# Optimization experiments

Hardware: AMD Instinct MI355X
Metric: run time of the kernel (lower is better)

## Reference

```python
import jax, jax.numpy as jnp
from jax import lax
import numpy as np

B, T = 64, 1024
N_MELS, ENC, DEC, LSTM, SPK = 80, 256, 128, 512, 256
CTX = ENC + SPK          # encoder_seq feature dim = 512
PRE = 2 * DEC            # prenet fc dims = 256
FILTERS, KS = 32, 31
MAX_R, R = 20, 1         # r buffer initialized to 1
DROP_P = 0.5


def _gru_cell(x, h, w_ih, w_hh, b_ih, b_hh):
    gi = x @ w_ih.T + b_ih
    gh = h @ w_hh.T + b_hh
    i_r, i_z, i_n = jnp.split(gi, 3, axis=-1)
    h_r, h_z, h_n = jnp.split(gh, 3, axis=-1)
    r = jax.nn.sigmoid(i_r + h_r)
    z = jax.nn.sigmoid(i_z + h_z)
    n = jnp.tanh(i_n + r * h_n)
    return (1.0 - z) * n + z * h


def _lstm_cell(x, h, c, w_ih, w_hh, b_ih, b_hh):
    g = x @ w_ih.T + h @ w_hh.T + b_ih + b_hh
    i, f, gg, o = jnp.split(g, 4, axis=-1)
    c2 = jax.nn.sigmoid(f) * c + jax.nn.sigmoid(i) * jnp.tanh(gg)
    h2 = jax.nn.sigmoid(o) * jnp.tanh(c2)
    return h2, c2


def setup_inputs() -> dict:
    key = jax.random.key(0)
    ks = jax.random.split(key, 40)
    n = lambda i, shp: jax.random.normal(ks[i], shp, jnp.float32)
    p = lambda i, shp: jax.random.normal(ks[i], shp, jnp.float32) * 0.05
    return {
        "encoder_seq": n(0, (B, T, CTX)),
        "encoder_seq_proj": n(1, (B, T, DEC)),
        "prenet_in": n(2, (B, N_MELS)),
        "attn_hidden": n(3, (B, DEC)),
        "rnn1_hidden": n(4, (B, LSTM)),
        "rnn2_hidden": n(5, (B, LSTM)),
        "rnn1_cell": n(6, (B, LSTM)),
        "rnn2_cell": n(7, (B, LSTM)),
        "context_vec": n(8, (B, CTX)),
        "chars": jax.random.randint(ks[9], (B, T), 0, 100),
        "t": 0,
        # LSA params (torch layout: Linear weight [out,in])
        "conv_w": p(10, (FILTERS, 1, KS)),
        "conv_b": p(11, (FILTERS,)),
        "L_w": p(12, (DEC, FILTERS)),
        "W_w": p(13, (DEC, DEC)),
        "W_b": p(14, (DEC,)),
        "v_w": p(15, (1, DEC)),
        # PreNet
        "fc1_w": p(16, (PRE, N_MELS)),
        "fc1_b": p(17, (PRE,)),
        "fc2_w": p(18, (PRE, PRE)),
        "fc2_b": p(19, (PRE,)),
        # GRUCell: in = CTX + PRE = 768, hidden = DEC
        "gru_w_ih": p(20, (3 * DEC, CTX + PRE)),
        "gru_w_hh": p(21, (3 * DEC, DEC)),
        "gru_b_ih": p(22, (3 * DEC,)),
        "gru_b_hh": p(23, (3 * DEC,)),
        # rnn_input Linear: CTX + DEC = 640 -> LSTM
        "ri_w": p(24, (LSTM, CTX + DEC)),
        "ri_b": p(25, (LSTM,)),
        # LSTMCells
        "l1_w_ih": p(26, (4 * LSTM, LSTM)),
        "l1_w_hh": p(27, (4 * LSTM, LSTM)),
        "l1_b_ih": p(28, (4 * LSTM,)),
        "l1_b_hh": p(29, (4 * LSTM,)),
        "l2_w_ih": p(30, (4 * LSTM, LSTM)),
        "l2_w_hh": p(31, (4 * LSTM, LSTM)),
        "l2_b_ih": p(32, (4 * LSTM,)),
        "l2_b_hh": p(33, (4 * LSTM,)),
        # output projections
        "mp_w": p(34, (N_MELS * MAX_R, LSTM)),
        "sp_w": p(35, (1, CTX + LSTM)),
        "sp_b": p(36, (1,)),
    }


def reference(encoder_seq, encoder_seq_proj, prenet_in, attn_hidden, rnn1_hidden,
              rnn2_hidden, rnn1_cell, rnn2_cell, context_vec, chars, t,
              conv_w, conv_b, L_w, W_w, W_b, v_w,
              fc1_w, fc1_b, fc2_w, fc2_b,
              gru_w_ih, gru_w_hh, gru_b_ih, gru_b_hh,
              ri_w, ri_b,
              l1_w_ih, l1_w_hh, l1_b_ih, l1_b_hh,
              l2_w_ih, l2_w_hh, l2_b_ih, l2_b_hh,
              mp_w, sp_w, sp_b):
    # PreNet (dropout always on, deterministic keys)
    dk1, dk2 = jax.random.split(jax.random.key(42))
    keep = 1.0 - DROP_P
    h = jax.nn.relu(prenet_in @ fc1_w.T + fc1_b)
    h = h * jax.random.bernoulli(dk1, keep, h.shape).astype(h.dtype) / keep
    h = jax.nn.relu(h @ fc2_w.T + fc2_b)
    prenet_out = h * jax.random.bernoulli(dk2, keep, h.shape).astype(h.dtype) / keep

    # attention GRU
    attn_h = _gru_cell(jnp.concatenate([context_vec, prenet_out], axis=-1),
                       attn_hidden, gru_w_ih, gru_w_hh, gru_b_ih, gru_b_hh)

    # LSA attention at t == 0 (cumulative attention is zeros)
    pq = attn_h @ W_w.T + W_b                              # [B, DEC]
    cumulative = jnp.zeros((B, 1, T), encoder_seq.dtype)
    loc = lax.conv_general_dilated(cumulative, conv_w, (1,), [((KS - 1) // 2,) * 2],
                                   dimension_numbers=("NCH", "OIH", "NCH"))
    loc = loc + conv_b[None, :, None]                      # [B, F, T]
    ploc = jnp.swapaxes(loc, 1, 2) @ L_w.T                 # [B, T, DEC]
    u = (jnp.tanh(pq[:, None, :] + encoder_seq_proj + ploc) @ v_w.T)[..., 0]  # [B, T]
    u = u * (chars != 0).astype(u.dtype)
    scores = jax.nn.softmax(u, axis=1)                     # [B, T]
    context = jnp.einsum("bt,btd->bd", scores, encoder_seq)  # [B, CTX]

    # residual LSTM stack (inference: no zoneout)
    x = jnp.concatenate([context, attn_h], axis=1) @ ri_w.T + ri_b
    h1, c1 = _lstm_cell(x, rnn1_hidden, rnn1_cell, l1_w_ih, l1_w_hh, l1_b_ih, l1_b_hh)
    x = x + h1
    h2, c2 = _lstm_cell(x, rnn2_hidden, rnn2_cell, l2_w_ih, l2_w_hh, l2_b_ih, l2_b_hh)
    x = x + h2

    mels = (x @ mp_w.T).reshape(B, N_MELS, MAX_R)[:, :, :R]  # [B, n_mels, r]
    stop = jax.nn.sigmoid(jnp.concatenate([x, context], axis=1) @ sp_w.T + sp_b)
    return mels, scores[:, None, :], attn_h, h1, h2, c1, c2, context, stop
```

## Files before the change

kernel.cpp:

```cpp
#include <hip/hip_runtime.h>
#include <stdint.h>

#define JAX_PARTITIONABLE 1
#define NB 512

__device__ __forceinline__ float tanh_f(float x) {
  float e = __expf(2.0f * x);
  return 1.0f - 2.0f / (e + 1.0f);
}
__device__ __forceinline__ float sigm(float x) {
  return 1.0f / (1.0f + __expf(-x));
}

__device__ __forceinline__ void stw(float* p, float v) {
  __hip_atomic_store(p, v, __ATOMIC_RELAXED, __HIP_MEMORY_SCOPE_AGENT);
}
__device__ __forceinline__ void stw4(float* p, float4 v) {
  union { float2 f; uint64_t u; } a, b;
  a.f.x = v.x; a.f.y = v.y; b.f.x = v.z; b.f.y = v.w;
  __hip_atomic_store((uint64_t*)p, a.u, __ATOMIC_RELAXED, __HIP_MEMORY_SCOPE_AGENT);
  __hip_atomic_store(((uint64_t*)p) + 1, b.u, __ATOMIC_RELAXED, __HIP_MEMORY_SCOPE_AGENT);
}

__device__ __forceinline__ void tf2x32(unsigned k0, unsigned k1, unsigned x0, unsigned x1,
                                       unsigned &o0, unsigned &o1) {
  unsigned ks0 = k0, ks1 = k1, ks2 = k0 ^ k1 ^ 0x1BD11BDAu;
  x0 += ks0; x1 += ks1;
#define RR(r) { x0 += x1; x1 = (x1 << r) | (x1 >> (32 - r)); x1 ^= x0; }
  RR(13) RR(15) RR(26) RR(6)  x0 += ks1; x1 += ks2 + 1u;
  RR(17) RR(29) RR(16) RR(24) x0 += ks2; x1 += ks0 + 2u;
  RR(13) RR(15) RR(26) RR(6)  x0 += ks0; x1 += ks1 + 3u;
  RR(17) RR(29) RR(16) RR(24) x0 += ks1; x1 += ks2 + 4u;
  RR(13) RR(15) RR(26) RR(6)  x0 += ks2; x1 += ks0 + 5u;
#undef RR
  o0 = x0; o1 = x1;
}

__device__ __forceinline__ float drop_scale(unsigned k0, unsigned k1, unsigned flat) {
#if JAX_PARTITIONABLE
  unsigned o0, o1; tf2x32(k0, k1, 0u, flat, o0, o1);
  unsigned bits = o0 ^ o1;
#else
  unsigned o0, o1, bits;
  if (flat < 8192u) { tf2x32(k0, k1, flat, flat + 8192u, o0, o1); bits = o0; }
  else             { tf2x32(k0, k1, flat - 8192u, flat, o0, o1); bits = o1; }
#endif
  return (bits >> 31) ? 0.0f : 2.0f;
}
__device__ __forceinline__ void get_drop_keys(unsigned &a0, unsigned &a1,
                                              unsigned &b0, unsigned &b1) {
#if JAX_PARTITIONABLE
  tf2x32(0u, 42u, 0u, 0u, a0, a1);
  tf2x32(0u, 42u, 0u, 1u, b0, b1);
#else
  unsigned p0, q0, p1, q1;
  tf2x32(0u, 42u, 0u, 2u, p0, q0);
  tf2x32(0u, 42u, 1u, 3u, p1, q1);
  a0 = p0; a1 = p1; b0 = q0; b1 = q1;
#endif
}

__device__ __forceinline__ void gbar(int* ibase, int phase) {
  __syncthreads();
  if (threadIdx.x == 0) {
    const int s = (int)(blockIdx.x & 15);
    int* sub   = ibase + s * 64;
    int* top   = ibase + 1024;
    int* flags = ibase + 1088;
    int old = __hip_atomic_fetch_add(sub, 1, __ATOMIC_RELAXED, __HIP_MEMORY_SCOPE_AGENT);
    if (old == phase * 32 - 1) {
      int t = __hip_atomic_fetch_add(top, 1, __ATOMIC_RELAXED, __HIP_MEMORY_SCOPE_AGENT);
      if (t == phase * 16 - 1) {
        #pragma unroll
        for (int i = 0; i < 16; i++)
          __hip_atomic_store(flags + i * 64, phase, __ATOMIC_RELAXED, __HIP_MEMORY_SCOPE_AGENT);
      }
    }
    long long guard = 0;
    while (__hip_atomic_load(flags + s * 64, __ATOMIC_RELAXED, __HIP_MEMORY_SCOPE_AGENT) < phase) {
      __builtin_amdgcn_s_sleep(4);
      if (++guard > (1LL << 21)) break;
    }
  }
  __syncthreads();
}

__global__ void k0(int* cnt) {
  for (int i = threadIdx.x; i < 2112; i += 256) cnt[i] = 0;
}

__global__ __launch_bounds__(256, 2) void kM(
    const float* es, const float* esp, const float* prenet_in,
    const float* rnn1_hidden, const float* rnn2_hidden,
    const float* rnn1_cell, const float* rnn2_cell,
    const float* context_vec, const float* attn_hidden, const int* chars,
    const float* conv_b, const float* L_w, const float* W_w, const float* W_b, const float* v_w,
    const float* fc1_w, const float* fc1_b, const float* fc2_w, const float* fc2_b,
    const float* gru_w_ih, const float* gru_w_hh, const float* gru_b_ih, const float* gru_b_hh,
    const float* ri_w, const float* ri_b,
    const float* l1_w_ih, const float* l1_w_hh, const float* l1_b_ih, const float* l1_b_hh,
    const float* l2_w_ih, const float* l2_w_hh, const float* l2_b_ih, const float* l2_b_hh,
    const float* mp_w, const float* sp_w, const float* sp_b,
    float* ws,
    float* mels_o, float* scores_o, float* attn_o, float* h1_o, float* h2_o,
    float* c1_o, float* c2_o, float* ctx_o, float* stop_o) {
  int* ibase = (int*)ws;
  float* pqc    = ws + 2112;
  float* phq    = ws + 2240;
  float* poq    = ws + 18624;
  float* ahq_h  = ws + 35008;
  float* u_buf  = ws + 43200;
  float* ctxq   = ws + 108736;
  float* xq     = ws + 141504;
  float* x2q    = ws + 174272;
  float* x3q    = ws + 207040;
  float* hq1    = ws + 239808;
  float* hq2    = ws + 272576;
  float* cvq    = ws + 305344;
  float* ahq_in = ws + 338112;
  float* c1pT   = ws + 346304;
  float* c2pT   = ws + 379072;

  const float4* cvq4   = (const float4*)cvq;
  const float4* phq4   = (const float4*)phq;
  const float4* poq4   = (const float4*)poq;
  const float4* ahq_in4= (const float4*)ahq_in;
  const float4* ahq_h4 = (const float4*)ahq_h;
  const float4* ctxq4  = (const float4*)ctxq;
  const float4* xq4    = (const float4*)xq;
  const float4* x2q4   = (const float4*)x2q;
  const float4* x3q4   = (const float4*)x3q;
  const float4* hq14   = (const float4*)hq1;
  const float4* hq24   = (const float4*)hq2;

  const int g = blockIdx.x, tid = threadIdx.x;
  const int w = tid >> 6, lane = tid & 63;
  __shared__ float sh[16640];

  if (g < 64) {
    for (int i = tid; i < 5120; i += 256) sh[(i / 80) * 81 + (i % 80)] = prenet_in[i];
    __syncthreads();
    unsigned d1k0, d1k1, d2k0, d2k1;
    get_drop_keys(d1k0, d1k1, d2k0, d2k1);
    const int j = g * 4 + w;
    float acc = fc1_b[j];
    const float* wr = fc1_w + j * 80;
    #pragma unroll 8
    for (int k = 0; k < 80; k += 2) {
      float2 wv = *(const float2*)(wr + k);
      acc += sh[lane * 81 + k] * wv.x + sh[lane * 81 + k + 1] * wv.y;
    }
    acc = fmaxf(acc, 0.0f) * drop_scale(d1k0, d1k1, (unsigned)(lane * 256 + j));
    stw(&phq[g * 256 + lane * 4 + w], acc);
  } else if (g < 96) {
    int t = (g - 64) * 256 + tid;
    int k4 = t >> 6, b = t & 63;
    stw4(&hq1[k4 * 256 + b * 4], ((const float4*)rnn1_hidden)[b * 128 + k4]);
  } else if (g < 128) {
    int t = (g - 96) * 256 + tid;
    int k4 = t >> 6, b = t & 63;
    stw4(&hq2[k4 * 256 + b * 4], ((const float4*)rnn2_hidden)[b * 128 + k4]);
  } else if (g < 160) {
    int t = (g - 128) * 256 + tid;
    int k4 = t >> 6, b = t & 63;
    stw4(&cvq[k4 * 256 + b * 4], ((const float4*)context_vec)[b * 128 + k4]);
  } else if (g < 168) {
    int t = (g - 160) * 256 + tid;
    int k4 = t >> 6, b = t & 63;
    stw4(&ahq_in[k4 * 256 + b * 4], ((const float4*)attn_hidden)[b * 32 + k4]);
  } else if (g < 232) {
    int base = (g - 168) * 512;
    #pragma unroll
    for (int e = 0; e < 2; e++) { int i = base + tid + e * 256; stw(&c1pT[i], rnn1_cell[(i & 63) * 512 + (i >> 6)]); }
  } else if (g < 296) {
    int base = (g - 232) * 512;
    #pragma unroll
    for (int e = 0; e < 2; e++) { int i = base + tid + e * 256; stw(&c2pT[i], rnn2_cell[(i & 63) * 512 + (i >> 6)]); }
  } else if (g < 360) {
    int base = (g - 296) * 512;
    #pragma unroll
    for (int e = 0; e < 2; e++) stw(&ctxq[base + tid + e * 256], 0.0f);
  } else if (g == 360) {
    if (tid < 128) {
      float acc = W_b[tid];
      const float* lw = L_w + tid * 32;
      #pragma unroll
      for (int f = 0; f < 32; f++) acc += conv_b[f] * lw[f];
      stw(&pqc[tid], acc);
    }
  } else {
    const unsigned wi0 = (unsigned)((g - 361) * 256 + tid);
    float acc = 0.0f;
    #pragma unroll
    for (int s = 0; s < 10; s++) acc += es[(size_t)(wi0 + (unsigned)s * 38656u) * 32];
    asm volatile("" :: "v"(acc));
  }
  gbar(ibase, 1);

  if (g < 64) {
    const int j = g * 4 + w;
    ((float4*)(sh + w * 256))[lane] = ((const float4*)(fc2_w + j * 256))[lane];
    __syncthreads();
    unsigned d1k0, d1k1, d2k0, d2k1;
    get_drop_keys(d1k0, d1k1, d2k0, d2k1);
    const float4* wv4 = (const float4*)(sh + w * 256);
    float acc = fc2_b[j];
    #pragma unroll 8
    for (int k4 = 0; k4 < 64; k4++) {
      float4 x4 = phq4[k4 * 64 + lane];
      float4 wv = wv4[k4];
      acc += x4.x * wv.x + x4.y * wv.y + x4.z * wv.z + x4.w * wv.w;
    }
    acc = fmaxf(acc, 0.0f) * drop_scale(d2k0, d2k1, (unsigned)(lane * 256 + j));
    stw(&poq[g * 256 + lane * 4 + w], acc);
  } else {
    const unsigned wi0 = (unsigned)((g - 64) * 256 + tid);
    float acc = 0.0f;
    #pragma unroll
    for (int s = 0; s < 6; s++) {
      unsigned idx = 386560u + wi0 + (unsigned)s * 114688u;
      if (idx < 1048576u) acc += es[(size_t)idx * 32];
    }
    asm volatile("" :: "v"(acc));
  }
  gbar(ibase, 2);

  if (g < 128) {
    if (w < 3) {
      const int rj = g + 128 * w;
      const float4* src = (const float4*)(gru_w_ih + (size_t)rj * 768);
      float4* dst = (float4*)(sh + w * 768);
      #pragma unroll
      for (int q = 0; q < 3; q++) dst[q * 64 + lane] = src[q * 64 + lane];
    } else {
      float4* dst = (float4*)(sh + 2304);
      if (lane < 32) {
        dst[lane]      = ((const float4*)gru_w_hh)[(size_t)g * 32 + lane];
        dst[32 + lane] = ((const float4*)gru_w_hh)[(size_t)(128 + g) * 32 + lane];
        dst[64 + lane] = ((const float4*)gru_w_hh)[(size_t)(256 + g) * 32 + lane];
      }
    }
    __syncthreads();
    if (w < 3) {
      const int rj = g + 128 * w;
      const float4* wv4 = (const float4*)(sh + w * 768);
      float acc = gru_b_ih[rj];
      #pragma unroll 4
      for (int k4 = 0; k4 < 128; k4++) {
        float4 x4 = cvq4[k4 * 64 + lane];
        float4 wv = wv4[k4];
        acc += x4.x * wv.x + x4.y * wv.y + x4.z * wv.z + x4.w * wv.w;
      }
      #pragma unroll 4
      for (int k4 = 0; k4 < 64; k4++) {
        float4 x4 = poq4[k4 * 64 + lane];
        float4 wv = wv4[128 + k4];
        acc += x4.x * wv.x + x4.y * wv.y + x4.z * wv.z + x4.w * wv.w;
      }
      sh[2688 + w * 64 + lane] = acc;
    } else {
      const float4* wh4 = (const float4*)(sh + 2304);
      #pragma unroll
      for (int r = 0; r < 3; r++) {
        float acc = gru_b_hh[r * 128 + g];
        #pragma unroll 4
        for (int k4 = 0; k4 < 32; k4++) {
          float4 x4 = ahq_in4[k4 * 64 + lane];
          float4 wv = wh4[r * 32 + k4];
          acc += x4.x * wv.x + x4.y * wv.y + x4.z * wv.z + x4.w * wv.w;
        }
        sh[2688 + (3 + r) * 64 + lane] = acc;
      }
    }
    __syncthreads();
    if (tid < 64) {
      float gr = sh[2688 + tid]       + sh[2688 + 192 + tid];
      float gz = sh[2688 + 64 + tid]  + sh[2688 + 256 + tid];
      float gin = sh[2688 + 128 + tid];
      float ghn = sh[2688 + 320 + tid];
      float a0 = ahq_in[(g >> 2) * 256 + tid * 4 + (g & 3)];
      float r = sigm(gr), z = sigm(gz);
      float h = (1.0f - z) * tanh_f(gin + r * ghn) + z * a0;
      stw(&ahq_h[(g >> 2) * 256 + tid * 4 + (g & 3)], h);
      attn_o[tid * 128 + g] = h;
    }
  } else {
    const unsigned wi0 = (unsigned)((g - 128) * 256 + tid);
    float acc = 0.0f;
    #pragma unroll
    for (int s = 0; s < 3; s++) {
      unsigned idx = wi0 + (unsigned)s * 98304u;
      if (idx < 262144u) acc += esp[(size_t)idx * 32];
    }
    if (g == 128) { if (tid < 512) acc += W_w[tid * 32]; }
    if (g == 129) {
      #pragma unroll
      for (int s = 0; s < 8; s++) acc += (float)chars[(tid + s * 256) * 32];
    }
    asm volatile("" :: "v"(acc));
  }
  gbar(ibase, 3);

  {
    const int b = g >> 3, tch = g & 7;
    {
      const float4* src = ((const float4*)W_w) + (size_t)(w * 32) * 32;
      float4* dst = (float4*)sh + w * 1024;
      #pragma unroll
      for (int q = 0; q < 16; q++) dst[q * 64 + lane] = src[q * 64 + lane];
    }
    float* pqs = sh + 16384;
    float* shh = sh + 16512;
    if (tid < 128) shh[tid] = ahq_h[(tid >> 2) * 256 + b * 4 + (tid & 3)];
    __syncthreads();
    float2 a2; a2.x = shh[2 * lane]; a2.y = shh[2 * lane + 1];
    for (int ni = 0; ni < 32; ni++) {
      int n = w * 32 + ni;
      float2 wv2 = *(const float2*)(sh + w * 4096 + ni * 128 + 2 * lane);
      float s = a2.x * wv2.x + a2.y * wv2.y;
      for (int off = 32; off > 0; off >>= 1) s += __shfl_xor(s, off, 64);
      if (lane == 0) pqs[n] = s + pqc[n];
    }
    __syncthreads();
    float2 p = *(const float2*)(pqs + 2 * lane);
    float2 v2 = *(const float2*)(v_w + 2 * lane);
    const int tb = tch * 128 + w * 32;
    const float* erow = esp + ((size_t)b * 1024 + tb) * 128 + 2 * lane;
    for (int i2 = 0; i2 < 8; i2++) {
      const float* er = erow + (size_t)i2 * 512;
      float2 e0 = *(const float2*)(er);
      float2 e1 = *(const float2*)(er + 128);
      float2 e2 = *(const float2*)(er + 256);
      float2 e3 = *(const float2*)(er + 384);
      float s0 = v2.x * tanh_f(p.x + e0.x) + v2.y * tanh_f(p.y + e0.y);
      float s1 = v2.x * tanh_f(p.x + e1.x) + v2.y * tanh_f(p.y + e1.y);
      float s2 = v2.x * tanh_f(p.x + e2.x) + v2.y * tanh_f(p.y + e2.y);
      float s3 = v2.x * tanh_f(p.x + e3.x) + v2.y * tanh_f(p.y + e3.y);
      for (int off = 32; off > 0; off >>= 1) {
        s0 += __shfl_down(s0, off, 64);
        s1 += __shfl_down(s1, off, 64);
        s2 += __shfl_down(s2, off, 64);
        s3 += __shfl_down(s3, off, 64);
      }
      if (lane == 0) {
        int t = tb + i2 * 4;
        stw(&u_buf[b * 1024 + t],     (chars[b * 1024 + t]     != 0) ? s0 : 0.0f);
        stw(&u_buf[b * 1024 + t + 1], (chars[b * 1024 + t + 1] != 0) ? s1 : 0.0f);
        stw(&u_buf[b * 1024 + t + 2], (chars[b * 1024 + t + 2] != 0) ? s2 : 0.0f);
        stw(&u_buf[b * 1024 + t + 3], (chars[b * 1024 + t + 3] != 0) ? s3 : 0.0f);
      }
    }
  }
  gbar(ibase, 4);

  {
    const int b = g >> 3, tch = g & 7;
    float* redm = sh;
    float* sc   = sh + 256;
    float* red4 = sh + 384;
    float4 uv = *(const float4*)(u_buf + b * 1024 + tid * 4);
    float m = fmaxf(fmaxf(uv.x, uv.y), fmaxf(uv.z, uv.w));
    redm[tid] = m;
    __syncthreads();
    for (int s = 128; s > 0; s >>= 1) { if (tid < s) redm[tid] = fmaxf(redm[tid], redm[tid + s]); __syncthreads(); }
    float M = redm[0];
    __syncthreads();
    float e0 = __expf(uv.x - M), e1 = __expf(uv.y - M), e2 = __expf(uv.z - M), e3 = __expf(uv.w - M);
    redm[tid] = e0 + e1 + e2 + e3;
    __syncthreads();
    for (int s = 128; s > 0; s >>= 1) { if (tid < s) redm[tid] += redm[tid + s]; __syncthreads(); }
    float inv = 1.0f / redm[0];
    if (tch == 0) {
      float4 r; r.x = e0 * inv; r.y = e1 * inv; r.z = e2 * inv; r.w = e3 * inv;
      *(float4*)(scores_o + b * 1024 + tid * 4) = r;
    }
    if (tid < 128) sc[tid] = __expf(u_buf[b * 1024 + tch * 128 + tid] - M) * inv;
    __syncthreads();
    float acc0 = 0, acc1 = 0, acc2 = 0, acc3 = 0, acc4 = 0, acc5 = 0, acc6 = 0, acc7 = 0;
    const float* base = es + ((size_t)b * 1024 + tch * 128) * 512 + lane * 8;
    for (int i = 0; i < 32; i += 2) {
      int t1 = 4 * i + w, t2 = t1 + 4;
      float4 wa1 = *(const float4*)(base + (size_t)t1 * 512);
      float4 wb1 = *(const float4*)(base + (size_t)t1 * 512 + 4);
      float4 wa2 = *(const float4*)(base + (size_t)t2 * 512);
      float4 wb2 = *(const float4*)(base + (size_t)t2 * 512 + 4);
      float s1 = sc[t1], s2 = sc[t2];
      acc0 += s1 * wa1.x + s2 * wa2.x; acc1 += s1 * wa1.y + s2 * wa2.y;
      acc2 += s1 * wa1.z + s2 * wa2.z; acc3 += s1 * wa1.w + s2 * wa2.w;
      acc4 += s1 * wb1.x + s2 * wb2.x; acc5 += s1 * wb1.y + s2 * wb2.y;
      acc6 += s1 * wb1.z + s2 * wb2.z; acc7 += s1 * wb1.w + s2 * wb2.w;
    }
    float* rr = red4 + w * 512 + lane * 8;
    rr[0] = acc0; rr[1] = acc1; rr[2] = acc2; rr[3] = acc3;
    rr[4] = acc4; rr[5] = acc5; rr[6] = acc6; rr[7] = acc7;
    __syncthreads();
    int d0 = tid * 2;
    float r0 = red4[d0] + red4[512 + d0] + red4[1024 + d0] + red4[1536 + d0];
    float r1 = red4[d0 + 1] + red4[512 + d0 + 1] + red4[1024 + d0 + 1] + red4[1536 + d0 + 1];
    atomicAdd(&ctxq[(d0 >> 2) * 256 + b * 4 + (d0 & 3)], r0);
    atomicAdd(&ctxq[((d0 + 1) >> 2) * 256 + b * 4 + ((d0 + 1) & 3)], r1);
  }
  gbar(ibase, 5);

  {
    const int n = g;
    if (tid < 160) ((float4*)sh)[tid] = ((const float4*)(ri_w + (size_t)n * 640))[tid];
    if (tid < 64) ctx_o[tid * 512 + n] = ctxq[(n >> 2) * 256 + tid * 4 + (n & 3)];
    __syncthreads();
    float acc = 0.0f;
    for (int k4 = w * 40; k4 < w * 40 + 40; k4++) {
      float4 wv = ((float4*)sh)[k4];
      float4 x4 = (k4 < 128) ? ctxq4[k4 * 64 + lane] : ahq_h4[(k4 - 128) * 64 + lane];
      acc += x4.x * wv.x + x4.y * wv.y + x4.z * wv.z + x4.w * wv.w;
    }
    sh[640 + w * 64 + lane] = acc;
    __syncthreads();
    if (tid < 64) stw(&xq[(n >> 2) * 256 + tid * 4 + (n & 3)],
                      ri_b[n] + sh[640 + tid] + sh[704 + tid] + sh[768 + tid] + sh[832 + tid]);
  }
  gbar(ibase, 6);

  {
    const int n = g + (w << 9);
    {
      const float4* si = (const float4*)(l1_w_ih + (size_t)n * 512);
      const float4* sh4 = (const float4*)(l1_w_hh + (size_t)n * 512);
      float4* di = (float4*)sh + w * 256;
      float4* dh = di + 128;
      #pragma unroll
      for (int q = 0; q < 2; q++) { di[q * 64 + lane] = si[q * 64 + lane]; dh[q * 64 + lane] = sh4[q * 64 + lane]; }
    }
    __syncthreads();
    const float4* di = (const float4*)sh + w * 256;
    const float4* dh = di + 128;
    float acc = l1_b_ih[n] + l1_b_hh[n];
    #pragma unroll 4
    for (int k4 = 0; k4 < 128; k4++) {
      float4 x4 = xq4[k4 * 64 + lane];
      float4 wv = di[k4];
      acc += x4.x * wv.x + x4.y * wv.y + x4.z * wv.z + x4.w * wv.w;
    }
    #pragma unroll 4
    for (int k4 = 0; k4 < 128; k4++) {
      float4 x4 = hq14[k4 * 64 + lane];
      float4 wv = dh[k4];
      acc += x4.x * wv.x + x4.y * wv.y + x4.z * wv.z + x4.w * wv.w;
    }
    sh[4096 + w * 64 + lane] = acc;
    __syncthreads();
    if (tid < 64) {
      float gi = sh[4096 + tid], gf = sh[4160 + tid], gg = sh[4224 + tid], go = sh[4288 + tid];
      float c = c1pT[g * 64 + tid];
      float c2 = sigm(gf) * c + sigm(gi) * tanh_f(gg);
      float h2v = sigm(go) * tanh_f(c2);
      h1_o[tid * 512 + g] = h2v;
      c1_o[tid * 512 + g] = c2;
      stw(&x2q[(g >> 2) * 256 + tid * 4 + (g & 3)],
          xq[(g >> 2) * 256 + tid * 4 + (g & 3)] + h2v);
    }
  }
  gbar(ibase, 7);

  {
    const int n = g + (w << 9);
    {
      const float4* si = (const float4*)(l2_w_ih + (size_t)n * 512);
      const float4* sh4 = (const float4*)(l2_w_hh + (size_t)n * 512);
      float4* di = (float4*)sh + w * 256;
      float4* dh = di + 128;
      #pragma unroll
      for (int q = 0; q < 2; q++) { di[q * 64 + lane] = si[q * 64 + lane]; dh[q * 64 + lane] = sh4[q * 64 + lane]; }
    }
    __syncthreads();
    const float4* di = (const float4*)sh + w * 256;
    const float4* dh = di + 128;
    float acc = l2_b_ih[n] + l2_b_hh[n];
    #pragma unroll 4
    for (int k4 = 0; k4 < 128; k4++) {
      float4 x4 = x2q4[k4 * 64 + lane];
      float4 wv = di[k4];
      acc += x4.x * wv.x + x4.y * wv.y + x4.z * wv.z + x4.w * wv.w;
    }
    #pragma unroll 4
    for (int k4 = 0; k4 < 128; k4++) {
      float4 x4 = hq24[k4 * 64 + lane];
      float4 wv = dh[k4];
      acc += x4.x * wv.x + x4.y * wv.y + x4.z * wv.z + x4.w * wv.w;
    }
    sh[4096 + w * 64 + lane] = acc;
    __syncthreads();
    if (tid < 64) {
      float gi = sh[4096 + tid], gf = sh[4160 + tid], gg = sh[4224 + tid], go = sh[4288 + tid];
      float c = c2pT[g * 64 + tid];
      float c2 = sigm(gf) * c + sigm(gi) * tanh_f(gg);
      float h2v = sigm(go) * tanh_f(c2);
      h2_o[tid * 512 + g] = h2v;
      c2_o[tid * 512 + g] = c2;
      stw(&x3q[(g >> 2) * 256 + tid * 4 + (g & 3)],
          x2q[(g >> 2) * 256 + tid * 4 + (g & 3)] + h2v);
    }
  }
  gbar(ibase, 8);

  if (g < 80) {
    const int m = g;
    if (tid < 128) ((float4*)sh)[tid] = ((const float4*)(mp_w + (size_t)m * 20 * 512))[tid];
    __syncthreads();
    float acc = 0.0f;
    for (int k4 = w * 32; k4 < w * 32 + 32; k4++) {
      float4 x4 = x3q4[k4 * 64 + lane];
      float4 wv = ((float4*)sh)[k4];
      acc += x4.x * wv.x + x4.y * wv.y + x4.z * wv.z + x4.w * wv.w;
    }
    sh[512 + w * 64 + lane] = acc;
    __syncthreads();
    if (tid < 64) mels_o[tid * 80 + m] = sh[512 + tid] + sh[576 + tid] + sh[640 + tid] + sh[704 + tid];
  } else if (g == 80) {
    ((float4*)sh)[tid] = ((const float4*)sp_w)[tid];
    __syncthreads();
    float acc = 0.0f;
    for (int k4 = w * 32; k4 < w * 32 + 32; k4++) {
      float4 x4 = x3q4[k4 * 64 + lane];
      float4 c4 = ctxq4[k4 * 64 + lane];
      float4 w1 = ((float4*)sh)[k4];
      float4 w2 = ((float4*)sh)[128 + k4];
      acc += x4.x * w1.x + x4.y * w1.y + x4.z * w1.z + x4.w * w1.w;
      acc += c4.x * w2.x + c4.y * w2.y + c4.z * w2.z + c4.w * w2.w;
    }
    sh[1024 + w * 64 + lane] = acc;
    __syncthreads();
    if (tid < 64) stop_o[tid] = sigm(sp_b[0] + sh[1024 + tid] + sh[1088 + tid] + sh[1152 + tid] + sh[1216 + tid]);
  }
}

extern "C" void kernel_launch(void* const* d_in, const int* in_sizes, int n_in,
                              void* d_out, int out_size, void* d_ws, size_t ws_size,
                              hipStream_t stream) {
  const float* es          = (const float*)d_in[0];
  const float* esp         = (const float*)d_in[1];
  const float* prenet_in   = (const float*)d_in[2];
  const float* attn_hidden = (const float*)d_in[3];
  const float* rnn1_hidden = (const float*)d_in[4];
  const float* rnn2_hidden = (const float*)d_in[5];
  const float* rnn1_cell   = (const float*)d_in[6];
  const float* rnn2_cell   = (const float*)d_in[7];
  const float* context_vec = (const float*)d_in[8];
  const int* chars         = (const int*)d_in[9];
  const float* conv_b = (const float*)d_in[12];
  const float* L_w    = (const float*)d_in[13];
  const float* W_w    = (const float*)d_in[14];
  const float* W_b    = (const float*)d_in[15];
  const float* v_w    = (const float*)d_in[16];
  const float* fc1_w  = (const float*)d_in[17];
  const float* fc1_b  = (const float*)d_in[18];
  const float* fc2_w  = (const float*)d_in[19];
  const float* fc2_b  = (const float*)d_in[20];
  const float* gru_w_ih = (const float*)d_in[21];
  const float* gru_w_hh = (const float*)d_in[22];
  const float* gru_b_ih = (const float*)d_in[23];
  const float* gru_b_hh = (const float*)d_in[24];
  const float* ri_w   = (const float*)d_in[25];
  const float* ri_b   = (const float*)d_in[26];
  const float* l1_w_ih = (const float*)d_in[27];
  const float* l1_w_hh = (const float*)d_in[28];
  const float* l1_b_ih = (const float*)d_in[29];
  const float* l1_b_hh = (const float*)d_in[30];
  const float* l2_w_ih = (const float*)d_in[31];
  const float* l2_w_hh = (const float*)d_in[32];
  const float* l2_b_ih = (const float*)d_in[33];
  const float* l2_b_hh = (const float*)d_in[34];
  const float* mp_w = (const float*)d_in[35];
  const float* sp_w = (const float*)d_in[36];
  const float* sp_b = (const float*)d_in[37];

  float* out = (float*)d_out;
  float* ws = (float*)d_ws;

  float* mels_o   = out + 0;
  float* scores_o = out + 5120;
  float* attn_o   = out + 70656;
  float* h1_o     = out + 78848;
  float* h2_o     = out + 111616;
  float* c1_o     = out + 144384;
  float* c2_o     = out + 177152;
  float* ctx_o    = out + 209920;
  float* stop_o   = out + 242688;

  k0<<<1, 256, 0, stream>>>((int*)ws);
  kM<<<NB, 256, 0, stream>>>(es, esp, prenet_in, rnn1_hidden, rnn2_hidden,
                             rnn1_cell, rnn2_cell, context_vec, attn_hidden, chars,
                             conv_b, L_w, W_w, W_b, v_w,
                             fc1_w, fc1_b, fc2_w, fc2_b,
                             gru_w_ih, gru_w_hh, gru_b_ih, gru_b_hh,
                             ri_w, ri_b,
                             l1_w_ih, l1_w_hh, l1_b_ih, l1_b_hh,
                             l2_w_ih, l2_w_hh, l2_b_ih, l2_b_hh,
                             mp_w, sp_w, sp_b,
                             ws,
                             mels_o, scores_o, attn_o, h1_o, h2_o,
                             c1_o, c2_o, ctx_o, stop_o);
}
```

Before: 425.6 us.

## Double persistent grid to 1024 blocks and rebalance attention and prefetch work

Raises the persistent kernel from 512 to 1024 blocks (4 per CU via launch bounds), widening the hierarchical grid barrier to 32 sub-counters and shrinking shared memory so occupancy fits. The attention score and context phases split each batch row across 16 blocks instead of 8, and the query projection is computed per-thread from global weights instead of a shared-memory staged warp reduction. Idle blocks' cache-warming loads are redistributed to touch LSTM, GRU and projection weights and encoder data earlier. The risk is more barrier traffic per phase and many idle blocks in the LSTM phases.

New measurement: 432.7 us. About the same (+1.7%).

```diff
diff --git a/kernel.cpp b/kernel.cpp
--- a/kernel.cpp
+++ b/kernel.cpp
@@ -2,7 +2,7 @@
 #include <stdint.h>
 
 #define JAX_PARTITIONABLE 1
-#define NB 512
+#define NB 1024
 
 __device__ __forceinline__ float tanh_f(float x) {
   float e = __expf(2.0f * x);
@@ -63,16 +63,16 @@
 __device__ __forceinline__ void gbar(int* ibase, int phase) {
   __syncthreads();
   if (threadIdx.x == 0) {
-    const int s = (int)(blockIdx.x & 15);
+    const int s = (int)(blockIdx.x & 31);
     int* sub   = ibase + s * 64;
-    int* top   = ibase + 1024;
-    int* flags = ibase + 1088;
+    int* top   = ibase + 2048;
+    int* flags = ibase + 2112;
     int old = __hip_atomic_fetch_add(sub, 1, __ATOMIC_RELAXED, __HIP_MEMORY_SCOPE_AGENT);
     if (old == phase * 32 - 1) {
       int t = __hip_atomic_fetch_add(top, 1, __ATOMIC_RELAXED, __HIP_MEMORY_SCOPE_AGENT);
-      if (t == phase * 16 - 1) {
+      if (t == phase * 32 - 1) {
         #pragma unroll
-        for (int i = 0; i < 16; i++)
+        for (int i = 0; i < 32; i++)
           __hip_atomic_store(flags + i * 64, phase, __ATOMIC_RELAXED, __HIP_MEMORY_SCOPE_AGENT);
       }
     }
@@ -86,10 +86,10 @@
 }
 
 __global__ void k0(int* cnt) {
-  for (int i = threadIdx.x; i < 2112; i += 256) cnt[i] = 0;
-}
-
-__global__ __launch_bounds__(256, 2) void kM(
+  for (int i = threadIdx.x; i < 4160; i += 256) cnt[i] = 0;
+}
+
+__global__ __launch_bounds__(256, 4) void kM(
     const float* es, const float* esp, const float* prenet_in,
     const float* rnn1_hidden, const float* rnn2_hidden,
     const float* rnn1_cell, const float* rnn2_cell,
@@ -105,21 +105,21 @@
     float* mels_o, float* scores_o, float* attn_o, float* h1_o, float* h2_o,
     float* c1_o, float* c2_o, float* ctx_o, float* stop_o) {
   int* ibase = (int*)ws;
-  float* pqc    = ws + 2112;
-  float* phq    = ws + 2240;
-  float* poq    = ws + 18624;
-  float* ahq_h  = ws + 35008;
-  float* u_buf  = ws + 43200;
-  float* ctxq   = ws + 108736;
-  float* xq     = ws + 141504;
-  float* x2q    = ws + 174272;
-  float* x3q    = ws + 207040;
-  float* hq1    = ws + 239808;
-  float* hq2    = ws + 272576;
-  float* cvq    = ws + 305344;
-  float* ahq_in = ws + 338112;
-  float* c1pT   = ws + 346304;
-  float* c2pT   = ws + 379072;
+  float* pqc    = ws + 4160;
+  float* phq    = ws + 4288;
+  float* poq    = ws + 20672;
+  float* ahq_h  = ws + 37056;
+  float* u_buf  = ws + 45248;
+  float* ctxq   = ws + 110784;
+  float* xq     = ws + 143552;
+  float* x2q    = ws + 176320;
+  float* x3q    = ws + 209088;
+  float* hq1    = ws + 241856;
+  float* hq2    = ws + 274624;
+  float* cvq    = ws + 307392;
+  float* ahq_in = ws + 340160;
+  float* c1pT   = ws + 348352;
+  float* c2pT   = ws + 381120;
 
   const float4* cvq4   = (const float4*)cvq;
   const float4* phq4   = (const float4*)phq;
@@ -135,7 +135,7 @@
 
   const int g = blockIdx.x, tid = threadIdx.x;
   const int w = tid >> 6, lane = tid & 63;
-  __shared__ float sh[16640];
+  __shared__ float sh[5440];
 
   if (g < 64) {
     for (int i = tid; i < 5120; i += 256) sh[(i / 80) * 81 + (i % 80)] = prenet_in[i];
@@ -192,7 +192,7 @@
     const unsigned wi0 = (unsigned)((g - 361) * 256 + tid);
     float acc = 0.0f;
     #pragma unroll
-    for (int s = 0; s < 10; s++) acc += es[(size_t)(wi0 + (unsigned)s * 38656u) * 32];
+    for (int s = 0; s < 4; s++) acc += es[(size_t)(wi0 + (unsigned)s * 169728u) * 32];
     asm volatile("" :: "v"(acc));
   }
   gbar(ibase, 1);
@@ -214,13 +214,23 @@
     acc = fmaxf(acc, 0.0f) * drop_scale(d2k0, d2k1, (unsigned)(lane * 256 + j));
     stw(&poq[g * 256 + lane * 4 + w], acc);
   } else {
-    const unsigned wi0 = (unsigned)((g - 64) * 256 + tid);
+    const unsigned wid = (unsigned)((g - 64) * 256 + tid);
     float acc = 0.0f;
-    #pragma unroll
-    for (int s = 0; s < 6; s++) {
-      unsigned idx = 386560u + wi0 + (unsigned)s * 114688u;
-      if (idx < 1048576u) acc += es[(size_t)idx * 32];
-    }
+    acc += esp[(size_t)wid * 32];
+    if (wid < 16384u) acc += esp[(size_t)(wid + 245760u) * 32];
+    if (wid < 32768u) {
+      acc += l1_w_ih[(size_t)wid * 32];
+      acc += l1_w_hh[(size_t)wid * 32];
+      acc += l2_w_ih[(size_t)wid * 32];
+      acc += l2_w_hh[(size_t)wid * 32];
+    }
+    if (wid < 10240u) acc += ri_w[(size_t)wid * 32];
+    if (wid < 9216u)  acc += gru_w_ih[(size_t)wid * 32];
+    if (wid < 1536u)  acc += gru_w_hh[(size_t)wid * 32];
+    if (wid < 512u)   acc += W_w[(size_t)wid * 32];
+    if (wid < 2048u)  acc += (float)chars[(size_t)wid * 32];
+    if (wid < 1280u)  acc += mp_w[(size_t)(wid >> 4) * 10240 + (wid & 15) * 32];
+    if (wid < 32u)    acc += sp_w[(size_t)wid * 32];
     asm volatile("" :: "v"(acc));
   }
   gbar(ibase, 2);
@@ -285,48 +295,37 @@
       attn_o[tid * 128 + g] = h;
     }
   } else {
-    const unsigned wi0 = (unsigned)((g - 128) * 256 + tid);
+    const unsigned wid = (unsigned)((g - 128) * 256 + tid);
     float acc = 0.0f;
-    #pragma unroll
-    for (int s = 0; s < 3; s++) {
-      unsigned idx = wi0 + (unsigned)s * 98304u;
-      if (idx < 262144u) acc += esp[(size_t)idx * 32];
-    }
-    if (g == 128) { if (tid < 512) acc += W_w[tid * 32]; }
-    if (g == 129) {
-      #pragma unroll
-      for (int s = 0; s < 8; s++) acc += (float)chars[(tid + s * 256) * 32];
-    }
+    acc += es[(size_t)(678912u + wid) * 32];
+    if (wid < 140288u) acc += es[(size_t)(908288u + wid) * 32];
     asm volatile("" :: "v"(acc));
   }
   gbar(ibase, 3);
 
   {
-    const int b = g >> 3, tch = g & 7;
-    {
-      const float4* src = ((const float4*)W_w) + (size_t)(w * 32) * 32;
-      float4* dst = (float4*)sh + w * 1024;
-      #pragma unroll
-      for (int q = 0; q < 16; q++) dst[q * 64 + lane] = src[q * 64 + lane];
-    }
-    float* pqs = sh + 16384;
-    float* shh = sh + 16512;
+    const int b = g >> 4, tch = g & 15;
+    float* shh = sh;
+    float* pqs = sh + 128;
     if (tid < 128) shh[tid] = ahq_h[(tid >> 2) * 256 + b * 4 + (tid & 3)];
     __syncthreads();
-    float2 a2; a2.x = shh[2 * lane]; a2.y = shh[2 * lane + 1];
-    for (int ni = 0; ni < 32; ni++) {
-      int n = w * 32 + ni;
-      float2 wv2 = *(const float2*)(sh + w * 4096 + ni * 128 + 2 * lane);
-      float s = a2.x * wv2.x + a2.y * wv2.y;
-      for (int off = 32; off > 0; off >>= 1) s += __shfl_xor(s, off, 64);
-      if (lane == 0) pqs[n] = s + pqc[n];
+    if (tid < 128) {
+      const int n = tid;
+      float acc = pqc[n];
+      const float4* wr = (const float4*)(W_w + n * 128);
+      #pragma unroll 8
+      for (int k4 = 0; k4 < 32; k4++) {
+        float4 wv = wr[k4];
+        acc += shh[k4 * 4] * wv.x + shh[k4 * 4 + 1] * wv.y + shh[k4 * 4 + 2] * wv.z + shh[k4 * 4 + 3] * wv.w;
+      }
+      pqs[n] = acc;
     }
     __syncthreads();
     float2 p = *(const float2*)(pqs + 2 * lane);
     float2 v2 = *(const float2*)(v_w + 2 * lane);
-    const int tb = tch * 128 + w * 32;
+    const int tb = tch * 64 + w * 16;
     const float* erow = esp + ((size_t)b * 1024 + tb) * 128 + 2 * lane;
-    for (int i2 = 0; i2 < 8; i2++) {
+    for (int i2 = 0; i2 < 4; i2++) {
       const float* er = erow + (size_t)i2 * 512;
       float2 e0 = *(const float2*)(er);
       float2 e1 = *(const float2*)(er + 128);
@@ -354,10 +353,10 @@
   gbar(ibase, 4);
 
   {
-    const int b = g >> 3, tch = g & 7;
+    const int b = g >> 4, tch = g & 15;
     float* redm = sh;
     float* sc   = sh + 256;
-    float* red4 = sh + 384;
+    float* red4 = sh + 320;
     float4 uv = *(const float4*)(u_buf + b * 1024 + tid * 4);
     float m = fmaxf(fmaxf(uv.x, uv.y), fmaxf(uv.z, uv.w));
     redm[tid] = m;
@@ -374,11 +373,11 @@
       float4 r; r.x = e0 * inv; r.y = e1 * inv; r.z = e2 * inv; r.w = e3 * inv;
       *(float4*)(scores_o + b * 1024 + tid * 4) = r;
     }
-    if (tid < 128) sc[tid] = __expf(u_buf[b * 1024 + tch * 128 + tid] - M) * inv;
+    if (tid < 64) sc[tid] = __expf(u_buf[b * 1024 + tch * 64 + tid] - M) * inv;
     __syncthreads();
     float acc0 = 0, acc1 = 0, acc2 = 0, acc3 = 0, acc4 = 0, acc5 = 0, acc6 = 0, acc7 = 0;
-    const float* base = es + ((size_t)b * 1024 + tch * 128) * 512 + lane * 8;
-    for (int i = 0; i < 32; i += 2) {
+    const float* base = es + ((size_t)b * 1024 + tch * 64) * 512 + lane * 8;
+    for (int i = 0; i < 16; i += 2) {
       int t1 = 4 * i + w, t2 = t1 + 4;
       float4 wa1 = *(const float4*)(base + (size_t)t1 * 512);
       float4 wb1 = *(const float4*)(base + (size_t)t1 * 512 + 4);
@@ -402,7 +401,7 @@
   }
   gbar(ibase, 5);
 
-  {
+  if (g < 512) {
     const int n = g;
     if (tid < 160) ((float4*)sh)[tid] = ((const float4*)(ri_w + (size_t)n * 640))[tid];
     if (tid < 64) ctx_o[tid * 512 + n] = ctxq[(n >> 2) * 256 + tid * 4 + (n & 3)];
@@ -420,7 +419,7 @@
   }
   gbar(ibase, 6);
 
-  {
+  if (g < 512) {
     const int n = g + (w << 9);
     {
       const float4* si = (const float4*)(l1_w_ih + (size_t)n * 512);
@@ -461,7 +460,7 @@
   }
   gbar(ibase, 7);
 
-  {
+  if (g < 512) {
     const int n = g + (w << 9);
     {
       const float4* si = (const float4*)(l2_w_ih + (size_t)n * 512);
```
